# Optimization experiments

Measured on AMD Instinct MI355X. Metric: run time of the kernel, lower is better.

Reference implementation:

```python
import jax, jax.numpy as jnp
import numpy as np

D_MODEL = 2048
N_HEADS = 16
D_HEAD = D_MODEL // N_HEADS  # 128
RANK = 32


def _orthogonal(key, rows, cols, dtype=jnp.float32):
    # mimic torch orthogonal init via QR
    a = jax.random.normal(key, (max(rows, cols), min(rows, cols)), dtype=jnp.float32)
    q, r = jnp.linalg.qr(a)
    q = q * jnp.sign(jnp.diagonal(r))
    if rows < cols:
        q = q.T
    return q.astype(dtype)


def setup_inputs() -> dict:
    key = jax.random.key(0)
    ks = jax.random.split(key, 8)
    B, T = 2, 2048
    x = jax.random.normal(ks[0], (B, T, D_MODEL), dtype=jnp.float32)
    s = 1.0 / np.sqrt(D_MODEL)
    Wq = jax.random.uniform(ks[1], (D_MODEL, D_MODEL), minval=-s, maxval=s, dtype=jnp.float32)
    Wk = jax.random.uniform(ks[2], (D_MODEL, D_MODEL), minval=-s, maxval=s, dtype=jnp.float32)
    Wv = jax.random.uniform(ks[3], (D_MODEL, D_MODEL), minval=-s, maxval=s, dtype=jnp.float32)
    Wo = jax.random.uniform(ks[4], (D_MODEL, D_MODEL), minval=-s, maxval=s, dtype=jnp.float32)
    # vein projector: project d_head -> rank, reconstruct rank -> d_head (orthogonal init)
    Wdown = _orthogonal(ks[5], D_HEAD, RANK)   # [d_head, r]
    Wup = _orthogonal(ks[6], RANK, D_HEAD)     # [r, d_head]
    return {"x": x, "Wq": Wq, "Wk": Wk, "Wv": Wv, "Wo": Wo, "Wdown": Wdown, "Wup": Wup}


def reference(x, Wq, Wk, Wv, Wo, Wdown, Wup):
    B, T, D = x.shape
    H, dh, r = N_HEADS, D_HEAD, RANK
    scale = 1.0 / np.sqrt(r)

    def heads(y):  # [B,T,D] -> [B,H,T,dh]
        return y.reshape(B, T, H, dh).transpose(0, 2, 1, 3)

    q = heads(x @ Wq.T)
    k = heads(x @ Wk.T)
    v = heads(x @ Wv.T)

    # project into vein (rank) space: [B,H,T,r]
    q_r = jnp.einsum('bhtd,dr->bhtr', q, Wdown)
    k_r = jnp.einsum('bhtd,dr->bhtr', k, Wdown)
    v_r = jnp.einsum('bhtd,dr->bhtr', v, Wdown)

    scores = jnp.einsum('bhqr,bhkr->bhqk', q_r, k_r) * scale  # [B,H,T,T]
    attn = jax.nn.softmax(scores, axis=-1)
    y_r = jnp.einsum('bhqk,bhkr->bhqr', attn, v_r)            # [B,H,T,r]
    y = jnp.einsum('bhtr,rd->bhtd', y_r, Wup)                  # reconstruct [B,H,T,dh]
    y = y.transpose(0, 2, 1, 3).reshape(B, T, D)
    out = y @ Wo.T
    return out
```

## Files before the change

### kernel.cpp

```cpp
#include <hip/hip_runtime.h>
#include <cstdint>
#include <cstddef>

typedef __bf16 bf16;
typedef __attribute__((ext_vector_type(8))) __bf16 bf16x8;
typedef __attribute__((ext_vector_type(4))) __bf16 bf16x4;
typedef __attribute__((ext_vector_type(2))) __bf16 bf16x2;
typedef __attribute__((ext_vector_type(4))) float f32x4;
typedef unsigned int u32;

#define D_MODEL 2048
#define QSCALE      0.17677669529663687f
#define QSCALE_L2E  (0.17677669529663687f * 1.4426950408889634f)

__device__ inline void async_load16(const void* gp, void* lp) {
  __builtin_amdgcn_global_load_lds(
      (const __attribute__((address_space(1))) u32*)gp,
      (__attribute__((address_space(3))) u32*)lp, 16, 0, 0);
}

__device__ inline float fast_exp2(float x) {
#if __has_builtin(__builtin_amdgcn_exp2f)
  return __builtin_amdgcn_exp2f(x);
#else
  return __expf(x * 0.6931471805599453f);
#endif
}

__global__ __launch_bounds__(256) void cvt_k(const float* __restrict__ x,
                                             bf16* __restrict__ xb) {
  const int i = (blockIdx.x * 256 + threadIdx.x) * 8;
  float4 a = *(const float4*)(x + i);
  float4 b = *(const float4*)(x + i + 4);
  bf16x8 o;
  o[0] = (bf16)a.x; o[1] = (bf16)a.y; o[2] = (bf16)a.z; o[3] = (bf16)a.w;
  o[4] = (bf16)b.x; o[5] = (bf16)b.y; o[6] = (bf16)b.z; o[7] = (bf16)b.w;
  *(bf16x8*)(xb + i) = o;
}

__global__ __launch_bounds__(256) void fold_qkv_k(
    const float* __restrict__ Wq, const float* __restrict__ Wk,
    const float* __restrict__ Wv, const float* __restrict__ Wdown,
    bf16* __restrict__ EffT) {
  __shared__ float wd[128][32];
  const int t = threadIdx.x;
  for (int i = t; i < 128 * 32; i += 256)
    ((float*)wd)[i] = Wdown[i];
  __syncthreads();
  const int mh = blockIdx.x;
  const float* W = (mh < 16) ? Wq : ((mh < 32) ? Wk : Wv);
  const int hrow = (mh & 15) * 128;
  const int d = blockIdx.y * 128 + (t & 127);
  const int rh = (t >> 7) * 16;
  float acc[16];
#pragma unroll
  for (int j = 0; j < 16; ++j) acc[j] = 0.f;
#pragma unroll 4
  for (int k = 0; k < 128; ++k) {
    float w = W[(size_t)(hrow + k) * D_MODEL + d];
    const float* wr = &wd[k][rh];
#pragma unroll
    for (int j = 0; j < 16; ++j) acc[j] += w * wr[j];
  }
  bf16* outp = EffT + (size_t)(mh * 32 + rh) * D_MODEL + d;
#pragma unroll
  for (int j = 0; j < 16; ++j) outp[(size_t)j * D_MODEL] = (bf16)acc[j];
}

__global__ __launch_bounds__(256) void fold_o_k(
    const bf16* __restrict__ Wob, const float* __restrict__ Wup,
    bf16* __restrict__ WoEffT) {
  __shared__ __align__(16) bf16 As_[128 * 128];
  __shared__ __align__(16) bf16 Bs_[32 * 128];
  const int t = threadIdx.x, wave = t >> 6, lane = t & 63;
  const int quad = lane >> 4, lc = lane & 15;
  const int d0 = blockIdx.x * 128, h = blockIdx.y;
#pragma unroll
  for (int a = 0; a < 8; ++a) {
    int r0 = wave * 32 + a * 4;
    int row = r0 + (lane >> 4);
    int g = (lane & 15) ^ (row & 15);
    async_load16(Wob + (size_t)(d0 + row) * 2048 + h * 128 + g * 8,
                 As_ + r0 * 128);
  }
  {
    int row = t >> 3;
    int c0 = (t & 7) * 2;
    const float* src = Wup + row * 128 + c0 * 8;
    float4 f0 = ((const float4*)src)[0], f1 = ((const float4*)src)[1];
    float4 f2 = ((const float4*)src)[2], f3 = ((const float4*)src)[3];
    bf16x8 b0, b1;
    b0[0] = (bf16)f0.x; b0[1] = (bf16)f0.y; b0[2] = (bf16)f0.z; b0[3] = (bf16)f0.w;
    b0[4] = (bf16)f1.x; b0[5] = (bf16)f1.y; b0[6] = (bf16)f1.z; b0[7] = (bf16)f1.w;
    b1[0] = (bf16)f2.x; b1[1] = (bf16)f2.y; b1[2] = (bf16)f2.z; b1[3] = (bf16)f2.w;
    b1[4] = (bf16)f3.x; b1[5] = (bf16)f3.y; b1[6] = (bf16)f3.z; b1[7] = (bf16)f3.w;
    *(bf16x8*)(Bs_ + row * 128 + ((c0 ^ (row & 15)) * 8)) = b0;
    *(bf16x8*)(Bs_ + row * 128 + (((c0 + 1) ^ (row & 15)) * 8)) = b1;
  }
  __syncthreads();
  f32x4 acc[2][2] = {};
  const int wm = wave * 32;
#pragma unroll
  for (int kc = 0; kc < 4; ++kc) {
    bf16x8 af[2], bfr[2];
#pragma unroll
    for (int mi = 0; mi < 2; ++mi) {
      int m = wm + mi * 16 + lc;
      af[mi] = *(const bf16x8*)(As_ + m * 128 + (((kc * 4 + quad) ^ (m & 15)) * 8));
    }
#pragma unroll
    for (int ni = 0; ni < 2; ++ni) {
      int n = ni * 16 + lc;
      bfr[ni] = *(const bf16x8*)(Bs_ + n * 128 + (((kc * 4 + quad) ^ (n & 15)) * 8));
    }
#pragma unroll
    for (int mi = 0; mi < 2; ++mi)
#pragma unroll
      for (int ni = 0; ni < 2; ++ni)
        acc[mi][ni] = __builtin_amdgcn_mfma_f32_16x16x32_bf16(
            af[mi], bfr[ni], acc[mi][ni], 0, 0, 0);
  }
#pragma unroll
  for (int mi = 0; mi < 2; ++mi)
#pragma unroll
    for (int ni = 0; ni < 2; ++ni)
#pragma unroll
      for (int reg = 0; reg < 4; ++reg)
        WoEffT[(size_t)(d0 + wm + mi * 16 + quad * 4 + reg) * 512 + h * 32 +
               ni * 16 + lc] = (bf16)acc[mi][ni][reg];
}

template <int EPI, int BM>
__global__ __launch_bounds__(256, (BM == 64 ? 3 : 2)) void gemm_bt_k(
    const bf16* __restrict__ A, const bf16* __restrict__ Bt,
    void* __restrict__ Cv, int M, int N, int K) {
  constexpr int MI = BM / 32;
  constexpr int AR = BM / 4;
  __shared__ __align__(16) bf16 As[2][BM * 64];
  __shared__ __align__(16) bf16 Bs[2][128 * 64];
  const int t = threadIdx.x, wave = t >> 6, lane = t & 63;
  const int quad = lane >> 4, lc = lane & 15;
  const size_t m0 = (size_t)blockIdx.x * BM;
  const size_t n0 = (size_t)blockIdx.y * 128;
  const int wm = (wave >> 1) * (MI * 16), wn = (wave & 1) * 64;
  const int sr = lane >> 3, ss = lane & 7;
  const bf16* Aga[MI]; const bf16* Bga[4]; int LoffA[MI], LoffB[4];
#pragma unroll
  for (int a = 0; a < MI; ++a) {
    int row = wave * AR + a * 8 + sr;
    Aga[a] = A + (m0 + row) * (size_t)K + (ss ^ (row & 7)) * 8;
    LoffA[a] = (wave * AR + a * 8) * 64;
  }
#pragma unroll
  for (int a = 0; a < 4; ++a) {
    int row = wave * 32 + a * 8 + sr;
    Bga[a] = Bt + (n0 + row) * (size_t)K + (ss ^ (row & 7)) * 8;
    LoffB[a] = (wave * 32 + a * 8) * 64;
  }
  f32x4 acc[MI][4] = {};
  const int NIT = K >> 6;
#pragma unroll
  for (int a = 0; a < MI; ++a) async_load16(Aga[a], &As[0][LoffA[a]]);
#pragma unroll
  for (int a = 0; a < 4; ++a) async_load16(Bga[a], &Bs[0][LoffB[a]]);
  __syncthreads();
  for (int it = 0; it < NIT; ++it) {
    const int cur = it & 1;
    if (it + 1 < NIT) {
      const int k0 = (it + 1) * 64;
#pragma unroll
      for (int a = 0; a < MI; ++a) async_load16(Aga[a] + k0, &As[1 - cur][LoffA[a]]);
#pragma unroll
      for (int a = 0; a < 4; ++a) async_load16(Bga[a] + k0, &Bs[1 - cur][LoffB[a]]);
    }
    const bf16* Asb = As[cur];
    const bf16* Bsb = Bs[cur];
#pragma unroll
    for (int kc = 0; kc < 2; ++kc) {
      bf16x8 af[MI], bfr[4];
#pragma unroll
      for (int mi = 0; mi < MI; ++mi) {
        int m = wm + mi * 16 + lc;
        af[mi] = *(const bf16x8*)(Asb + m * 64 + (((kc * 4 + quad) ^ (m & 7)) * 8));
      }
#pragma unroll
      for (int ni = 0; ni < 4; ++ni) {
        int n = wn + ni * 16 + lc;
        bfr[ni] = *(const bf16x8*)(Bsb + n * 64 + (((kc * 4 + quad) ^ (n & 7)) * 8));
      }
#pragma unroll
      for (int mi = 0; mi < MI; ++mi)
#pragma unroll
        for (int ni = 0; ni < 4; ++ni)
          acc[mi][ni] = __builtin_amdgcn_mfma_f32_16x16x32_bf16(
              af[mi], bfr[ni], acc[mi][ni], 0, 0, 0);
    }
    __syncthreads();
  }

  if (EPI == 0) {
    float* C = (float*)Cv;
#pragma unroll
    for (int mi = 0; mi < MI; ++mi)
#pragma unroll
      for (int ni = 0; ni < 4; ++ni) {
        size_t row = m0 + wm + mi * 16 + quad * 4;
        size_t col = n0 + wn + ni * 16 + lc;
#pragma unroll
        for (int reg = 0; reg < 4; ++reg)
          C[(row + reg) * (size_t)N + col] = acc[mi][ni][reg];
      }
  } else {
    bf16* C = (bf16*)Cv;
#pragma unroll
    for (int mi = 0; mi < MI; ++mi)
#pragma unroll
      for (int ni = 0; ni < 4; ++ni) {
        int n = (int)n0 + wn + ni * 16 + lc;
        int mat = n >> 9, hh = (n >> 5) & 15, r = n & 31;
        float sc = (mat == 0) ? QSCALE_L2E : 1.0f;
        int trow = (int)m0 + wm + mi * 16 + quad * 4;
        int b = trow >> 11, tl = trow & 2047;
        if (mat == 2) {
          int tile = tl >> 7, kin = tl & 127;
          size_t off = ((size_t)(b * 16 + hh) * 3 + 2) * 65536 +
                       (size_t)tile * 4096 + r * 128 +
                       (((kin >> 3) ^ (r & 15)) << 3) + (kin & 7);
          bf16x4 pk;
#pragma unroll
          for (int reg = 0; reg < 4; ++reg) pk[reg] = (bf16)acc[mi][ni][reg];
          *(bf16x4*)(C + off) = pk;
        } else {
#pragma unroll
          for (int reg = 0; reg < 4; ++reg) {
            size_t off = (((size_t)(b * 16 + hh) * 3 + mat) * 2048 + tl + reg) * 32 + r;
            C[off] = (bf16)(acc[mi][ni][reg] * sc);
          }
        }
      }
  }
}

__global__ __launch_bounds__(256, 4) void attn_k(const bf16* __restrict__ QKVr,
                                                 float* __restrict__ Op,
                                                 float* __restrict__ Sums) {
  const int bh = blockIdx.x, qb = blockIdx.y, kvh = blockIdx.z;
  const size_t base = (size_t)bh * 3 * 65536;
  const bf16* Q   = QKVr + base;
  const bf16* Kr  = Q + 65536 + (size_t)kvh * 1024 * 32;
  const bf16* Vrb = Q + 131072 + (size_t)kvh * 8 * 4096;
  __shared__ __align__(16) bf16 Ks[2][128 * 32];
  __shared__ __align__(16) bf16 Vt[2][32 * 128];
  __shared__ __align__(16) bf16 Ps[4 * 32 * 32];
  const int t = threadIdx.x, wave = t >> 6, lane = t & 63;
  const int quad = lane >> 4, lc = lane & 15;
  const int qbase = qb * 128 + wave * 32;
  const bf16x8 qf0 = *(const bf16x8*)(Q + (size_t)(qbase + lc) * 32 + quad * 8);
  const bf16x8 qf1 = *(const bf16x8*)(Q + (size_t)(qbase + 16 + lc) * 32 + quad * 8);
  f32x4 o00 = {}, o01 = {}, o10 = {}, o11 = {};
  f32x4 os0 = {}, os1 = {};
  bf16x8 ones;
#pragma unroll
  for (int j = 0; j < 8; ++j) ones[j] = (bf16)1.0f;
  const int krow = wave * 16 + (lane >> 2);
  const bf16* Kg = Kr + (size_t)krow * 32 + ((lane & 3) ^ ((krow >> 1) & 3)) * 8;
  bf16* pw = Ps + wave * 32 * 32;
  const int psw = (lc & 3) ^ (lc >> 2);

  async_load16(Kg, &Ks[0][wave * 16 * 32]);
  async_load16(Kg + (size_t)64 * 32, &Ks[0][(64 + wave * 16) * 32]);
  async_load16(Vrb + (wave * 2) * 512 + lane * 8, &Vt[0][(wave * 2) * 512]);
  async_load16(Vrb + (wave * 2 + 1) * 512 + lane * 8, &Vt[0][(wave * 2 + 1) * 512]);
  __syncthreads();

  for (int it = 0; it < 8; ++it) {
    const int kt = it * 128, cur = it & 1;
    if (it < 7) {
      async_load16(Kg + (size_t)(kt + 128) * 32, &Ks[1 - cur][wave * 16 * 32]);
      async_load16(Kg + (size_t)(kt + 192) * 32, &Ks[1 - cur][(64 + wave * 16) * 32]);
      const bf16* vg = Vrb + (size_t)(it + 1) * 4096;
      async_load16(vg + (wave * 2) * 512 + lane * 8, &Vt[1 - cur][(wave * 2) * 512]);
      async_load16(vg + (wave * 2 + 1) * 512 + lane * 8, &Vt[1 - cur][(wave * 2 + 1) * 512]);
    }
    const bf16* ksb = Ks[cur];
    const bf16* vtb = Vt[cur];
#pragma unroll
    for (int qtr = 0; qtr < 4; ++qtr) {
#pragma unroll
      for (int nii = 0; nii < 2; ++nii) {
        int ni = qtr * 2 + nii;
        int n = ni * 16 + lc;
        bf16x8 kf = *(const bf16x8*)(ksb + n * 32 + ((quad ^ ((n >> 1) & 3)) * 8));
        f32x4 z = {0.f, 0.f, 0.f, 0.f};
        f32x4 s0 = __builtin_amdgcn_mfma_f32_16x16x32_bf16(kf, qf0, z, 0, 0, 0);
        f32x4 s1 = __builtin_amdgcn_mfma_f32_16x16x32_bf16(kf, qf1, z, 0, 0, 0);
        bf16x4 p0, p1;
#pragma unroll
        for (int reg = 0; reg < 4; ++reg) {
          p0[reg] = (bf16)fast_exp2(s0[reg]);
          p1[reg] = (bf16)fast_exp2(s1[reg]);
        }
        int off = (((2 * nii + (quad >> 1)) ^ psw) * 8) + (quad & 1) * 4;
        *(bf16x4*)(pw + lc * 32 + off) = p0;
        *(bf16x4*)(pw + (16 + lc) * 32 + off) = p1;
      }
      int co = (quad ^ psw) * 8;
      bf16x8 pf0 = *(const bf16x8*)(pw + lc * 32 + co);
      bf16x8 pf1 = *(const bf16x8*)(pw + (16 + lc) * 32 + co);
      int vo = ((qtr * 4 + quad) ^ lc) * 8;
      bf16x8 v0 = *(const bf16x8*)(vtb + lc * 128 + vo);
      bf16x8 v1 = *(const bf16x8*)(vtb + (16 + lc) * 128 + vo);
      o00 = __builtin_amdgcn_mfma_f32_16x16x32_bf16(pf0, v0, o00, 0, 0, 0);
      o01 = __builtin_amdgcn_mfma_f32_16x16x32_bf16(pf0, v1, o01, 0, 0, 0);
      o10 = __builtin_amdgcn_mfma_f32_16x16x32_bf16(pf1, v0, o10, 0, 0, 0);
      o11 = __builtin_amdgcn_mfma_f32_16x16x32_bf16(pf1, v1, o11, 0, 0, 0);
      os0 = __builtin_amdgcn_mfma_f32_16x16x32_bf16(pf0, ones, os0, 0, 0, 0);
      os1 = __builtin_amdgcn_mfma_f32_16x16x32_bf16(pf1, ones, os1, 0, 0, 0);
    }
    __syncthreads();
  }
  const int b = bh >> 4, h = bh & 15;
  float* op = Op + (size_t)kvh * 4096 * 512;
#pragma unroll
  for (int reg = 0; reg < 4; ++reg) {
    size_t r0 = (size_t)b * 2048 + qbase + quad * 4 + reg;
    size_t r1 = r0 + 16;
    op[r0 * 512 + h * 32 + lc]      = o00[reg];
    op[r0 * 512 + h * 32 + 16 + lc] = o01[reg];
    op[r1 * 512 + h * 32 + lc]      = o10[reg];
    op[r1 * 512 + h * 32 + 16 + lc] = o11[reg];
  }
  if (lc == 0) {
    float* sp = Sums + (size_t)kvh * 65536 + (size_t)bh * 2048 + qbase;
#pragma unroll
    for (int reg = 0; reg < 4; ++reg) {
      sp[quad * 4 + reg]      = os0[reg];
      sp[16 + quad * 4 + reg] = os1[reg];
    }
  }
}

__global__ __launch_bounds__(256) void comb_k(const float* __restrict__ Op,
                                              const float* __restrict__ Sums,
                                              bf16* __restrict__ Yr) {
  const int idx = blockIdx.x * 256 + threadIdx.x;
  const int row = idx >> 6;
  const int c8 = (idx & 63) * 8;
  const int b = row >> 11, tl = row & 2047;
  const int h = c8 >> 5;
  const size_t si = (size_t)(b * 16 + h) * 2048 + tl;
  const float inv = 1.0f / (Sums[si] + Sums[65536 + si]);
  const float4* p0 = (const float4*)(Op + (size_t)row * 512 + c8);
  const float4* p1 = (const float4*)(Op + 4096 * 512 + (size_t)row * 512 + c8);
  float4 a0 = p0[0], a1 = p0[1];
  float4 b0 = p1[0], b1 = p1[1];
  bf16x8 o;
  o[0] = (bf16)((a0.x + b0.x) * inv); o[1] = (bf16)((a0.y + b0.y) * inv);
  o[2] = (bf16)((a0.z + b0.z) * inv); o[3] = (bf16)((a0.w + b0.w) * inv);
  o[4] = (bf16)((a1.x + b1.x) * inv); o[5] = (bf16)((a1.y + b1.y) * inv);
  o[6] = (bf16)((a1.z + b1.z) * inv); o[7] = (bf16)((a1.w + b1.w) * inv);
  *(bf16x8*)(Yr + (size_t)row * 512 + c8) = o;
}

extern "C" void kernel_launch(void* const* d_in, const int* in_sizes, int n_in,
                              void* d_out, int out_size, void* d_ws, size_t ws_size,
                              hipStream_t stream) {
  const float* x     = (const float*)d_in[0];
  const float* Wq    = (const float*)d_in[1];
  const float* Wk    = (const float*)d_in[2];
  const float* Wv    = (const float*)d_in[3];
  const float* Wo    = (const float*)d_in[4];
  const float* Wdown = (const float*)d_in[5];
  const float* Wup   = (const float*)d_in[6];
  float* out = (float*)d_out;

  char* ws = (char*)d_ws;
  bf16*  EffT   = (bf16*)(ws);
  float* Sums   = (float*)(ws);
  bf16*  WoEffT = (bf16*)(ws + 6291456);
  bf16*  QKVr   = (bf16*)(ws + 8388608);
  bf16*  Wob    = (bf16*)(ws + 8388608);
  bf16*  Yrb    = (bf16*)(ws + 20971520);
  bf16*  xb     = (bf16*)(ws + 25165824);
  float* Opart  = (float*)(ws + 25165824);

  cvt_k<<<dim3(4096), dim3(256), 0, stream>>>(x, xb);
  cvt_k<<<dim3(2048), dim3(256), 0, stream>>>(Wo, Wob);
  fold_qkv_k<<<dim3(48, 16), dim3(256), 0, stream>>>(Wq, Wk, Wv, Wdown, EffT);
  fold_o_k<<<dim3(16, 16), dim3(256), 0, stream>>>(Wob, Wup, WoEffT);
  gemm_bt_k<1, 64><<<dim3(64, 12), dim3(256), 0, stream>>>(xb, EffT, QKVr,
                                                           4096, 1536, 2048);
  attn_k<<<dim3(32, 16, 2), dim3(256), 0, stream>>>(QKVr, Opart, Sums);
  comb_k<<<dim3(1024), dim3(256), 0, stream>>>(Opart, Sums, Yrb);
  gemm_bt_k<0, 128><<<dim3(32, 16), dim3(256), 0, stream>>>(Yrb, WoEffT, out,
                                                            4096, 2048, 512);
}
```

Before: 241.1 us.

## Merge preprocessing kernels into one launch and fold Wo conversion into fold step

Replaces four preprocessing launches (x conversion, Wo conversion, QKV weight fold, output weight fold) with one kernel that dispatches on block index. The separate Wo-to-bf16 pass and its workspace buffer go away, and the output-fold blocks now read fp32 Wo directly and convert while staging into shared memory. This cuts launch overhead and a round trip of the converted Wo through memory. In exchange, every block reserves 40KB of shared memory, which may lower occupancy for the simple conversion blocks, and the fold of Wo loses its async global-to-LDS loads.

```diff
diff --git a/kernel.cpp b/kernel.cpp
--- a/kernel.cpp
+++ b/kernel.cpp
@@ -27,61 +27,71 @@
 #endif
 }
 
-__global__ __launch_bounds__(256) void cvt_k(const float* __restrict__ x,
-                                             bf16* __restrict__ xb) {
-  const int i = (blockIdx.x * 256 + threadIdx.x) * 8;
-  float4 a = *(const float4*)(x + i);
-  float4 b = *(const float4*)(x + i + 4);
-  bf16x8 o;
-  o[0] = (bf16)a.x; o[1] = (bf16)a.y; o[2] = (bf16)a.z; o[3] = (bf16)a.w;
-  o[4] = (bf16)b.x; o[5] = (bf16)b.y; o[6] = (bf16)b.z; o[7] = (bf16)b.w;
-  *(bf16x8*)(xb + i) = o;
-}
-
-__global__ __launch_bounds__(256) void fold_qkv_k(
-    const float* __restrict__ Wq, const float* __restrict__ Wk,
-    const float* __restrict__ Wv, const float* __restrict__ Wdown,
-    bf16* __restrict__ EffT) {
-  __shared__ float wd[128][32];
+__global__ __launch_bounds__(256) void prep_k(
+    const float* __restrict__ x,  const float* __restrict__ Wq,
+    const float* __restrict__ Wk, const float* __restrict__ Wv,
+    const float* __restrict__ Wo, const float* __restrict__ Wdown,
+    const float* __restrict__ Wup,
+    bf16* __restrict__ xb, bf16* __restrict__ EffT,
+    bf16* __restrict__ WoEffT) {
+  __shared__ __align__(16) char smem_[40960];
+  const int bid = blockIdx.x;
   const int t = threadIdx.x;
-  for (int i = t; i < 128 * 32; i += 256)
-    ((float*)wd)[i] = Wdown[i];
-  __syncthreads();
-  const int mh = blockIdx.x;
-  const float* W = (mh < 16) ? Wq : ((mh < 32) ? Wk : Wv);
-  const int hrow = (mh & 15) * 128;
-  const int d = blockIdx.y * 128 + (t & 127);
-  const int rh = (t >> 7) * 16;
-  float acc[16];
-#pragma unroll
-  for (int j = 0; j < 16; ++j) acc[j] = 0.f;
+
+  if (bid < 4096) {
+    const int i = (bid * 256 + t) * 8;
+    float4 a = *(const float4*)(x + i);
+    float4 b = *(const float4*)(x + i + 4);
+    bf16x8 o;
+    o[0] = (bf16)a.x; o[1] = (bf16)a.y; o[2] = (bf16)a.z; o[3] = (bf16)a.w;
+    o[4] = (bf16)b.x; o[5] = (bf16)b.y; o[6] = (bf16)b.z; o[7] = (bf16)b.w;
+    *(bf16x8*)(xb + i) = o;
+    return;
+  }
+
+  if (bid < 4864) {
+    float* wd = (float*)smem_;
+    for (int i = t; i < 128 * 32; i += 256) wd[i] = Wdown[i];
+    __syncthreads();
+    const int rel = bid - 4096;
+    const int mh = rel % 48;
+    const int dblk = rel / 48;
+    const float* W = (mh < 16) ? Wq : ((mh < 32) ? Wk : Wv);
+    const int hrow = (mh & 15) * 128;
+    const int d = dblk * 128 + (t & 127);
+    const int rh = (t >> 7) * 16;
+    float acc[16];
+#pragma unroll
+    for (int j = 0; j < 16; ++j) acc[j] = 0.f;
 #pragma unroll 4
-  for (int k = 0; k < 128; ++k) {
-    float w = W[(size_t)(hrow + k) * D_MODEL + d];
-    const float* wr = &wd[k][rh];
-#pragma unroll
-    for (int j = 0; j < 16; ++j) acc[j] += w * wr[j];
-  }
-  bf16* outp = EffT + (size_t)(mh * 32 + rh) * D_MODEL + d;
-#pragma unroll
-  for (int j = 0; j < 16; ++j) outp[(size_t)j * D_MODEL] = (bf16)acc[j];
-}
-
-__global__ __launch_bounds__(256) void fold_o_k(
-    const bf16* __restrict__ Wob, const float* __restrict__ Wup,
-    bf16* __restrict__ WoEffT) {
-  __shared__ __align__(16) bf16 As_[128 * 128];
-  __shared__ __align__(16) bf16 Bs_[32 * 128];
-  const int t = threadIdx.x, wave = t >> 6, lane = t & 63;
+    for (int k = 0; k < 128; ++k) {
+      float w = W[(size_t)(hrow + k) * D_MODEL + d];
+      const float* wr = wd + k * 32 + rh;
+#pragma unroll
+      for (int j = 0; j < 16; ++j) acc[j] += w * wr[j];
+    }
+    bf16* outp = EffT + (size_t)(mh * 32 + rh) * D_MODEL + d;
+#pragma unroll
+    for (int j = 0; j < 16; ++j) outp[(size_t)j * D_MODEL] = (bf16)acc[j];
+    return;
+  }
+
+  bf16* As_ = (bf16*)smem_;
+  bf16* Bs_ = (bf16*)(smem_ + 32768);
+  const int rel = bid - 4864;
+  const int d0 = (rel & 15) * 128, h = rel >> 4;
+  const int wave = t >> 6, lane = t & 63;
   const int quad = lane >> 4, lc = lane & 15;
-  const int d0 = blockIdx.x * 128, h = blockIdx.y;
 #pragma unroll
   for (int a = 0; a < 8; ++a) {
-    int r0 = wave * 32 + a * 4;
-    int row = r0 + (lane >> 4);
-    int g = (lane & 15) ^ (row & 15);
-    async_load16(Wob + (size_t)(d0 + row) * 2048 + h * 128 + g * 8,
-                 As_ + r0 * 128);
+    int cc = a * 256 + t;
+    int row = cc >> 4, c = cc & 15;
+    const float* src = Wo + (size_t)(d0 + row) * 2048 + h * 128 + c * 8;
+    float4 f0 = ((const float4*)src)[0], f1 = ((const float4*)src)[1];
+    bf16x8 v;
+    v[0] = (bf16)f0.x; v[1] = (bf16)f0.y; v[2] = (bf16)f0.z; v[3] = (bf16)f0.w;
+    v[4] = (bf16)f1.x; v[5] = (bf16)f1.y; v[6] = (bf16)f1.z; v[7] = (bf16)f1.w;
+    *(bf16x8*)(As_ + row * 128 + ((c ^ (row & 15)) * 8)) = v;
   }
   {
     int row = t >> 3;
@@ -379,15 +389,12 @@
   float* Sums   = (float*)(ws);
   bf16*  WoEffT = (bf16*)(ws + 6291456);
   bf16*  QKVr   = (bf16*)(ws + 8388608);
-  bf16*  Wob    = (bf16*)(ws + 8388608);
   bf16*  Yrb    = (bf16*)(ws + 20971520);
   bf16*  xb     = (bf16*)(ws + 25165824);
   float* Opart  = (float*)(ws + 25165824);
 
-  cvt_k<<<dim3(4096), dim3(256), 0, stream>>>(x, xb);
-  cvt_k<<<dim3(2048), dim3(256), 0, stream>>>(Wo, Wob);
-  fold_qkv_k<<<dim3(48, 16), dim3(256), 0, stream>>>(Wq, Wk, Wv, Wdown, EffT);
-  fold_o_k<<<dim3(16, 16), dim3(256), 0, stream>>>(Wob, Wup, WoEffT);
+  prep_k<<<dim3(5120), dim3(256), 0, stream>>>(x, Wq, Wk, Wv, Wo, Wdown, Wup,
+                                               xb, EffT, WoEffT);
   gemm_bt_k<1, 64><<<dim3(64, 12), dim3(256), 0, stream>>>(xb, EffT, QKVr,
                                                            4096, 1536, 2048);
   attn_k<<<dim3(32, 16, 2), dim3(256), 0, stream>>>(QKVr, Opart, Sums);
```

Measured after the change: 230.9 us. 4.2% less time.
